# Performance work log

Measured on AMD Instinct MI355X. Metric: run time of the kernel, lower is better.

Reference implementation:

```python
import jax, jax.numpy as jnp
import numpy as np

B, T, D, U = 32, 512, 512, 512  # batch, seq_len, input dim, lstm units


def setup_inputs() -> dict:
    key = jax.random.key(0)
    ks = jax.random.split(key, 8)
    s_in = 1.0 / np.sqrt(D)
    s_rec = 1.0 / np.sqrt(U)
    return {
        "x": jax.random.normal(ks[0], (B, T, D), dtype=jnp.float32),
        "z": jax.random.normal(ks[1], (B, U), dtype=jnp.float32) * 0.1,
        # forward-direction LSTM params (Keras gate order: i, f, c, o)
        "Wf": jax.random.normal(ks[2], (D, 4 * U), dtype=jnp.float32) * s_in,
        "Uf": jax.random.normal(ks[3], (U, 4 * U), dtype=jnp.float32) * s_rec,
        "bf": jnp.zeros((4 * U,), dtype=jnp.float32),
        # backward-direction LSTM params
        "Wb": jax.random.normal(ks[4], (D, 4 * U), dtype=jnp.float32) * s_in,
        "Ub": jax.random.normal(ks[5], (U, 4 * U), dtype=jnp.float32) * s_rec,
        "bb": jnp.zeros((4 * U,), dtype=jnp.float32),
    }


def _lstm(x, h0, c0, W, Uw, b, reverse):
    """Single-direction LSTM, return_sequences=True. Keras gate order i,f,c,o."""
    u = h0.shape[-1]
    # precompute input projections for all timesteps in one big GEMM
    xg = jnp.einsum("btd,dk->btk", x, W) + b  # [B,T,4U]

    def step(carry, xg_t):
        h, c = carry
        g = xg_t + h @ Uw  # [B,4U]
        i = jax.nn.sigmoid(g[:, :u])
        f = jax.nn.sigmoid(g[:, u:2 * u])
        cc = jnp.tanh(g[:, 2 * u:3 * u])
        o = jax.nn.sigmoid(g[:, 3 * u:])
        c = f * c + i * cc
        h = o * jnp.tanh(c)
        return (h, c), h

    # scan over time; reverse=True == Keras go_backwards + output re-reversal
    _, hs = jax.lax.scan(step, (h0, c0), jnp.swapaxes(xg, 0, 1), reverse=reverse)
    return jnp.swapaxes(hs, 0, 1)  # [B,T,U]


def reference(x, z, Wf, Uf, bf, Wb, Ub, bb):
    # conditional=True: initial_state = [z, z, z, z] -> both directions get (h0=z, c0=z)
    fwd = _lstm(x, z, z, Wf, Uf, bf, reverse=False)
    bwd = _lstm(x, z, z, Wb, Ub, bb, reverse=True)
    return fwd + bwd  # Bidirectional merge_mode='sum', return_sequences=True
```

## Files before the change

### kernel.cpp

```cpp
#include <hip/hip_runtime.h>
#include <hip/hip_bf16.h>


typedef __attribute__((ext_vector_type(8))) __bf16 bf16x8;
typedef __attribute__((ext_vector_type(4))) __bf16 bf16x4;
typedef __attribute__((ext_vector_type(4))) float fvec4;

#define AS_G(p) ((const __attribute__((address_space(1))) void*)(p))
#define AS_L(p) ((__attribute__((address_space(3))) void*)(p))

__device__ __forceinline__ float sigm(float x) {
  return __builtin_amdgcn_rcpf(1.f + __expf(-x));
}
__device__ __forceinline__ float tanh_f(float x) {
  return 1.f - 2.f * __builtin_amdgcn_rcpf(__expf(2.f * x) + 1.f);
}

__device__ __forceinline__ void st_h4(__bf16* p, float h0, float h1) {
  union { __bf16 h[2]; unsigned int u; } pk;
  pk.h[0] = (__bf16)h0;
  pk.h[1] = (__bf16)h1;
  __hip_atomic_store((unsigned int*)p, pk.u, __ATOMIC_RELAXED, __HIP_MEMORY_SCOPE_AGENT);
}


__global__ void k_convert_x(const float* __restrict__ x, __bf16* __restrict__ xb) {
  size_t i = ((size_t)blockIdx.x * 256 + threadIdx.x) * 8;
  fvec4 a = *(const fvec4*)(x + i);
  fvec4 b = *(const fvec4*)(x + i + 4);
  bf16x8 o;
#pragma unroll
  for (int j = 0; j < 4; ++j) { o[j] = (__bf16)a[j]; o[4 + j] = (__bf16)b[j]; }
  *(bf16x8*)(xb + i) = o;
}

__global__ void k_build_T(const float* __restrict__ src, const float* __restrict__ bvec,
                          __bf16* __restrict__ dst, float* __restrict__ bias_out) {
  int p = blockIdx.x;
  int g = p >> 6, r = p & 63, w = r >> 4, q = r & 15, jj = q >> 2, gate = q & 3;
  int orig = gate * 512 + g * 16 + w * 4 + jj;
  for (int k = threadIdx.x; k < 512; k += 256)
    dst[(size_t)p * 512 + k] = (__bf16)src[(size_t)k * 2048 + orig];
  if (bias_out && threadIdx.x == 0) bias_out[p] = bvec[orig];
}

__global__ void k_init_flags(int* mbox) {
  int i = blockIdx.x * 256 + threadIdx.x;
  if (i < 2048) mbox[i] = 0;
}

__global__ void k_init_h(const float* __restrict__ z, __bf16* __restrict__ hbuf) {
  int idx = blockIdx.x * 256 + threadIdx.x;
  int dir = idx >> 14, rem = idx & 16383;
  int ks = rem >> 10, row = (rem >> 5) & 31, c = rem & 31;
  hbuf[(size_t)dir * 32768 + rem] = (__bf16)z[row * 512 + ks * 32 + c];
}


__global__ __launch_bounds__(256, 2) void k_gemm_xw(
    const __bf16* __restrict__ A,
    const __bf16* __restrict__ Bt,
    const float* __restrict__ bias,
    __bf16* __restrict__ C)
{
  __shared__ __align__(16) __bf16 As[128 * 32];
  __shared__ __align__(16) __bf16 Bs[128 * 32];
  const int tid = threadIdx.x;
  const int w = tid >> 6, lane = tid & 63, quad = lane >> 4, l15 = lane & 15;
  const int m0 = blockIdx.y * 128, n0 = blockIdx.x * 128;
  const int wm = w & 1, wn = w >> 1;

  fvec4 acc[4][4];
  const fvec4 zero = {0.f, 0.f, 0.f, 0.f};
#pragma unroll
  for (int i = 0; i < 4; ++i)
#pragma unroll
    for (int j = 0; j < 4; ++j) acc[i][j] = zero;

  for (int kb = 0; kb < 16; ++kb) {
    const int k0 = kb * 32;
#pragma unroll
    for (int i = 0; i < 2; ++i) {
      const int c = (i * 4 + w) * 64 + lane;
      const int row = c >> 2, kk = (c & 3) * 8;
      __builtin_amdgcn_global_load_lds(AS_G(A + (size_t)(m0 + row) * 512 + k0 + kk),
                                       AS_L(As + (size_t)(i * 4 + w) * 512), 16, 0, 0);
      __builtin_amdgcn_global_load_lds(AS_G(Bt + (size_t)(n0 + row) * 512 + k0 + kk),
                                       AS_L(Bs + (size_t)(i * 4 + w) * 512), 16, 0, 0);
    }
    __syncthreads();
    bf16x8 af[4], bfr[4];
#pragma unroll
    for (int mt = 0; mt < 4; ++mt)
      af[mt] = *(const bf16x8*)(As + (wm * 64 + mt * 16 + l15) * 32 + quad * 8);
#pragma unroll
    for (int nt = 0; nt < 4; ++nt)
      bfr[nt] = *(const bf16x8*)(Bs + (wn * 64 + nt * 16 + l15) * 32 + quad * 8);
#pragma unroll
    for (int mt = 0; mt < 4; ++mt)
#pragma unroll
      for (int nt = 0; nt < 4; ++nt)
        acc[mt][nt] = __builtin_amdgcn_mfma_f32_16x16x32_bf16(af[mt], bfr[nt], acc[mt][nt], 0, 0, 0);
    __syncthreads();
  }

#pragma unroll
  for (int nt = 0; nt < 4; ++nt) {
    const int col = n0 + wn * 64 + nt * 16 + l15;
    const float bv = bias[col];
#pragma unroll
    for (int mt = 0; mt < 4; ++mt) {
      const int rowb = m0 + wm * 64 + mt * 16 + quad * 4;
#pragma unroll
      for (int r = 0; r < 4; ++r)
        C[(size_t)(rowb + r) * 4096 + col] = (__bf16)(acc[mt][nt][r] + bv);
    }
  }
}


__global__ __launch_bounds__(256, 1) void k_lstm_rec(
    const __bf16* __restrict__ xg,
    const float* __restrict__ z,
    const __bf16* __restrict__ UT,
    __bf16* __restrict__ hbuf,
    float* __restrict__ outf,
    __bf16* __restrict__ outb,
    int* __restrict__ mbox)
{
  const int blk = blockIdx.x, dir = blk >> 5, g = blk & 31;
  const int tid = threadIdx.x, w = tid >> 6, lane = tid & 63;
  const int quad = lane >> 4, l15 = lane & 15;
  __shared__ __align__(16) __bf16 h_lds[16384];
  __shared__ __align__(16) float gates[32][68];

  bf16x8 breg[16];
  {
    const __bf16* up = UT + ((size_t)dir * 2048 + g * 64 + w * 16 + l15) * 512 + quad * 8;
#pragma unroll
    for (int ks = 0; ks < 16; ++ks) breg[ks] = *(const bf16x8*)(up + ks * 32);
  }

  const int b = lane >> 1, jpair = lane & 1;
  const int hcol = g * 16 + w * 4 + jpair * 2;
  float c0 = z[b * 512 + hcol];
  float c1 = z[b * 512 + hcol + 1];
  const __bf16* hsrc = hbuf + (size_t)dir * 32768;
  const int stoff = (g >> 1) * 1024 + b * 32 + (g & 1) * 16 + w * 4 + jpair * 2;
  const int stage_off = w * 4096 + lane * 8;
  const int swz8 = ((lane & 3) ^ ((lane >> 3) & 3)) * 8;
  const int fr_swz = ((l15 >> 1) & 3);
  int* my_line = mbox + dir * 1024 + g * 32;
  int* my_col  = mbox + dir * 1024 + lane * 32 + g;
  const fvec4 zero = {0.f, 0.f, 0.f, 0.f};

  for (int kt = 0; kt < 512; ++kt) {
    const int t = dir ? (511 - kt) : kt;
    const int pr = kt & 1;

    const bf16x8 xv = *(const bf16x8*)(xg + (size_t)(b * 512 + t) * 4096 +
                                       dir * 2048 + g * 64 + w * 16 + jpair * 8);

    if (kt > 0) {
      if (w == 0) {
        const int* mb = my_line + (lane & 31);
        for (;;) {
          int v = __hip_atomic_load(mb, __ATOMIC_RELAXED, __HIP_MEMORY_SCOPE_AGENT);
          if (!__ballot(lane < 32 && v < kt)) break;
          __builtin_amdgcn_s_sleep(1);
        }
      }
      __syncthreads();
    }

    {
      const unsigned long long* src =
          (const unsigned long long*)(hsrc + pr * 16384 + stage_off);
      unsigned long long tmp[16];
#pragma unroll
      for (int it = 0; it < 8; ++it) {
        tmp[2 * it]     = __hip_atomic_load(src + it * 128,
                            __ATOMIC_RELAXED, __HIP_MEMORY_SCOPE_AGENT);
        tmp[2 * it + 1] = __hip_atomic_load(src + it * 128 + 1,
                            __ATOMIC_RELAXED, __HIP_MEMORY_SCOPE_AGENT);
      }
#pragma unroll
      for (int it = 0; it < 8; ++it) {
        union { unsigned long long u[2]; bf16x8 v; } cv;
        cv.u[0] = tmp[2 * it];
        cv.u[1] = tmp[2 * it + 1];
        *(bf16x8*)(h_lds + (w * 4 + (it >> 1)) * 1024 +
                   ((it & 1) * 16 + (lane >> 2)) * 32 + swz8) = cv.v;
      }
    }
    __syncthreads();

    fvec4 acc0 = zero, acc1 = zero;
#pragma unroll 8
    for (int ks = 0; ks < 16; ++ks) {
      bf16x8 a0 = *(const bf16x8*)(h_lds + ks * 1024 + l15 * 32 +
                                   ((quad ^ fr_swz) * 8));
      bf16x8 a1 = *(const bf16x8*)(h_lds + ks * 1024 + (16 + l15) * 32 +
                                   ((quad ^ fr_swz) * 8));
      acc0 = __builtin_amdgcn_mfma_f32_16x16x32_bf16(a0, breg[ks], acc0, 0, 0, 0);
      acc1 = __builtin_amdgcn_mfma_f32_16x16x32_bf16(a1, breg[ks], acc1, 0, 0, 0);
    }

#pragma unroll
    for (int r = 0; r < 4; ++r) {
      gates[quad * 4 + r][w * 16 + l15] = acc0[r];
      gates[16 + quad * 4 + r][w * 16 + l15] = acc1[r];
    }
    const fvec4 gA = *(const fvec4*)&gates[b][w * 16 + jpair * 8];
    const fvec4 gB = *(const fvec4*)&gates[b][w * 16 + jpair * 8 + 4];

    float xf[8];
#pragma unroll
    for (int j = 0; j < 8; ++j) xf[j] = (float)xv[j];

    float ii = sigm(gA[0] + xf[0]);
    float ff = sigm(gA[1] + xf[1]);
    float cc = tanh_f(gA[2] + xf[2]);
    float oo = sigm(gA[3] + xf[3]);
    c0 = ff * c0 + ii * cc;
    const float h0 = oo * tanh_f(c0);

    ii = sigm(gB[0] + xf[4]);
    ff = sigm(gB[1] + xf[5]);
    cc = tanh_f(gB[2] + xf[6]);
    oo = sigm(gB[3] + xf[7]);
    c1 = ff * c1 + ii * cc;
    const float h1 = oo * tanh_f(c1);

    st_h4(hbuf + (size_t)dir * 32768 + ((kt + 1) & 1) * 16384 + stoff, h0, h1);

    __syncthreads();
    if (w == 0 && lane < 32)
      __hip_atomic_store(my_col, kt + 1, __ATOMIC_RELAXED, __HIP_MEMORY_SCOPE_AGENT);

    const size_t oidx = (size_t)(b * 512 + t) * 512 + hcol;
    if (dir == 0) {
      outf[oidx] = h0;
      outf[oidx + 1] = h1;
    } else {
      outb[oidx] = (__bf16)h0;
      outb[oidx + 1] = (__bf16)h1;
    }
  }
}


__global__ void k_add_bwd(float* __restrict__ out, const __bf16* __restrict__ outb) {
  size_t i = ((size_t)blockIdx.x * 256 + threadIdx.x) * 4;
  if (i >= (size_t)32 * 512 * 512) return;
  fvec4 o = *(const fvec4*)(out + i);
  bf16x4 bv = *(const bf16x4*)(outb + i);
#pragma unroll
  for (int j = 0; j < 4; ++j) o[j] += (float)bv[j];
  *(fvec4*)(out + i) = o;
}


extern "C" void kernel_launch(void* const* d_in, const int* in_sizes, int n_in,
                              void* d_out, int out_size, void* d_ws, size_t ws_size,
                              hipStream_t stream) {
  const float* x  = (const float*)d_in[0];
  const float* z  = (const float*)d_in[1];
  const float* Wf = (const float*)d_in[2];
  const float* Uf = (const float*)d_in[3];
  const float* bf = (const float*)d_in[4];
  const float* Wb = (const float*)d_in[5];
  const float* Ub = (const float*)d_in[6];
  const float* bb = (const float*)d_in[7];
  float* out = (float*)d_out;
  char* ws = (char*)d_ws;

  size_t off = 0;
  __bf16* xg    = (__bf16*)(ws + off); off += (size_t)16384 * 4096 * 2;
  __bf16* UT    = (__bf16*)(ws + off); off += (size_t)2 * 2048 * 512 * 2;
  __bf16* hbuf  = (__bf16*)(ws + off); off += (size_t)2 * 2 * 16384 * 2;
  int*    mbox  = (int*)(ws + off);    off += 8192;
  float*  biasp = (float*)(ws + off);  off += 4096 * 4;
  char* uni = ws + off;
  __bf16* xb   = (__bf16*)uni;
  __bf16* WT   = (__bf16*)(uni + (size_t)16384 * 512 * 2);
  __bf16* outb = (__bf16*)uni;

  k_convert_x<<<4096, 256, 0, stream>>>(x, xb);
  k_build_T<<<2048, 256, 0, stream>>>(Wf, bf, WT, biasp);
  k_build_T<<<2048, 256, 0, stream>>>(Wb, bb, WT + (size_t)2048 * 512, biasp + 2048);
  k_build_T<<<2048, 256, 0, stream>>>(Uf, nullptr, UT, nullptr);
  k_build_T<<<2048, 256, 0, stream>>>(Ub, nullptr, UT + (size_t)2048 * 512, nullptr);
  k_init_flags<<<8, 256, 0, stream>>>(mbox);
  k_init_h<<<128, 256, 0, stream>>>(z, hbuf);
  k_gemm_xw<<<dim3(32, 128), 256, 0, stream>>>(xb, WT, biasp, xg);
  k_lstm_rec<<<64, 256, 0, stream>>>(xg, z, UT, hbuf, out, outb, mbox);
  k_add_bwd<<<8192, 256, 0, stream>>>(out, outb);
}
```

Measured before the change: 2.205 ms.

## Replace mailbox flag barrier with poison-value data-driven sync on triple-buffered h

Measured after the change: 2.667 ms. +21.0%, slower.

```diff
diff --git a/kernel.cpp b/kernel.cpp
--- a/kernel.cpp
+++ b/kernel.cpp
@@ -9,6 +9,8 @@
 #define AS_G(p) ((const __attribute__((address_space(1))) void*)(p))
 #define AS_L(p) ((__attribute__((address_space(3))) void*)(p))
 
+#define POISON32 0x7F807F80u
+
 __device__ __forceinline__ float sigm(float x) {
   return __builtin_amdgcn_rcpf(1.f + __expf(-x));
 }
@@ -16,11 +18,14 @@
   return 1.f - 2.f * __builtin_amdgcn_rcpf(__expf(2.f * x) + 1.f);
 }
 
+__device__ __forceinline__ void st_u32(unsigned int* p, unsigned int v) {
+  __hip_atomic_store(p, v, __ATOMIC_RELAXED, __HIP_MEMORY_SCOPE_AGENT);
+}
 __device__ __forceinline__ void st_h4(__bf16* p, float h0, float h1) {
   union { __bf16 h[2]; unsigned int u; } pk;
   pk.h[0] = (__bf16)h0;
   pk.h[1] = (__bf16)h1;
-  __hip_atomic_store((unsigned int*)p, pk.u, __ATOMIC_RELAXED, __HIP_MEMORY_SCOPE_AGENT);
+  st_u32((unsigned int*)p, pk.u);
 }
 
 
@@ -44,16 +49,14 @@
   if (bias_out && threadIdx.x == 0) bias_out[p] = bvec[orig];
 }
 
-__global__ void k_init_flags(int* mbox) {
-  int i = blockIdx.x * 256 + threadIdx.x;
-  if (i < 2048) mbox[i] = 0;
-}
-
 __global__ void k_init_h(const float* __restrict__ z, __bf16* __restrict__ hbuf) {
   int idx = blockIdx.x * 256 + threadIdx.x;
-  int dir = idx >> 14, rem = idx & 16383;
-  int ks = rem >> 10, row = (rem >> 5) & 31, c = rem & 31;
-  hbuf[(size_t)dir * 32768 + rem] = (__bf16)z[row * 512 + ks * 32 + c];
+  int dir = idx / 49152, rem = idx % 49152;
+  int slot = rem >> 14, e = rem & 16383;
+  int ks = e >> 10, row = (e >> 5) & 31, c = e & 31;
+  union { unsigned short u; __bf16 h; } pz; pz.u = 0x7F80;
+  hbuf[(size_t)dir * 49152 + rem] =
+      (slot == 0) ? (__bf16)z[row * 512 + ks * 32 + c] : pz.h;
 }
 
 
@@ -125,8 +128,7 @@
     const __bf16* __restrict__ UT,
     __bf16* __restrict__ hbuf,
     float* __restrict__ outf,
-    __bf16* __restrict__ outb,
-    int* __restrict__ mbox)
+    __bf16* __restrict__ outb)
 {
   const int blk = blockIdx.x, dir = blk >> 5, g = blk & 31;
   const int tid = threadIdx.x, w = tid >> 6, lane = tid & 63;
@@ -145,53 +147,52 @@
   const int hcol = g * 16 + w * 4 + jpair * 2;
   float c0 = z[b * 512 + hcol];
   float c1 = z[b * 512 + hcol + 1];
-  const __bf16* hsrc = hbuf + (size_t)dir * 32768;
+  __bf16* hbase = hbuf + (size_t)dir * 49152;
   const int stoff = (g >> 1) * 1024 + b * 32 + (g & 1) * 16 + w * 4 + jpair * 2;
   const int stage_off = w * 4096 + lane * 8;
   const int swz8 = ((lane & 3) ^ ((lane >> 3) & 3)) * 8;
   const int fr_swz = ((l15 >> 1) & 3);
-  int* my_line = mbox + dir * 1024 + g * 32;
-  int* my_col  = mbox + dir * 1024 + lane * 32 + g;
   const fvec4 zero = {0.f, 0.f, 0.f, 0.f};
 
   for (int kt = 0; kt < 512; ++kt) {
     const int t = dir ? (511 - kt) : kt;
-    const int pr = kt & 1;
+    const int slot_r = kt % 3, slot_w = (kt + 1) % 3, slot_p = (kt + 2) % 3;
 
     const bf16x8 xv = *(const bf16x8*)(xg + (size_t)(b * 512 + t) * 4096 +
                                        dir * 2048 + g * 64 + w * 16 + jpair * 8);
 
-    if (kt > 0) {
-      if (w == 0) {
-        const int* mb = my_line + (lane & 31);
-        for (;;) {
-          int v = __hip_atomic_load(mb, __ATOMIC_RELAXED, __HIP_MEMORY_SCOPE_AGENT);
-          if (!__ballot(lane < 32 && v < kt)) break;
-          __builtin_amdgcn_s_sleep(1);
-        }
-      }
-      __syncthreads();
-    }
-
+    unsigned long long tmp[16];
     {
       const unsigned long long* src =
-          (const unsigned long long*)(hsrc + pr * 16384 + stage_off);
-      unsigned long long tmp[16];
-#pragma unroll
-      for (int it = 0; it < 8; ++it) {
-        tmp[2 * it]     = __hip_atomic_load(src + it * 128,
-                            __ATOMIC_RELAXED, __HIP_MEMORY_SCOPE_AGENT);
-        tmp[2 * it + 1] = __hip_atomic_load(src + it * 128 + 1,
-                            __ATOMIC_RELAXED, __HIP_MEMORY_SCOPE_AGENT);
-      }
-#pragma unroll
-      for (int it = 0; it < 8; ++it) {
-        union { unsigned long long u[2]; bf16x8 v; } cv;
-        cv.u[0] = tmp[2 * it];
-        cv.u[1] = tmp[2 * it + 1];
-        *(bf16x8*)(h_lds + (w * 4 + (it >> 1)) * 1024 +
-                   ((it & 1) * 16 + (lane >> 2)) * 32 + swz8) = cv.v;
-      }
+          (const unsigned long long*)(hbase + slot_r * 16384 + stage_off);
+      bool dirty;
+      do {
+#pragma unroll
+        for (int it = 0; it < 8; ++it) {
+          tmp[2 * it]     = __hip_atomic_load(src + it * 128,
+                              __ATOMIC_RELAXED, __HIP_MEMORY_SCOPE_AGENT);
+          tmp[2 * it + 1] = __hip_atomic_load(src + it * 128 + 1,
+                              __ATOMIC_RELAXED, __HIP_MEMORY_SCOPE_AGENT);
+        }
+        dirty = false;
+#pragma unroll
+        for (int j = 0; j < 16; ++j) {
+          dirty |= ((unsigned int)tmp[j] == POISON32);
+          dirty |= ((unsigned int)(tmp[j] >> 32) == POISON32);
+        }
+      } while (dirty);
+    }
+
+    if (kt < 511)
+      st_u32((unsigned int*)(hbase + slot_p * 16384 + stoff), POISON32);
+
+#pragma unroll
+    for (int it = 0; it < 8; ++it) {
+      union { unsigned long long u[2]; bf16x8 v; } cv;
+      cv.u[0] = tmp[2 * it];
+      cv.u[1] = tmp[2 * it + 1];
+      *(bf16x8*)(h_lds + (w * 4 + (it >> 1)) * 1024 +
+                 ((it & 1) * 16 + (lane >> 2)) * 32 + swz8) = cv.v;
     }
     __syncthreads();
 
@@ -232,11 +233,8 @@
     c1 = ff * c1 + ii * cc;
     const float h1 = oo * tanh_f(c1);
 
-    st_h4(hbuf + (size_t)dir * 32768 + ((kt + 1) & 1) * 16384 + stoff, h0, h1);
-
-    __syncthreads();
-    if (w == 0 && lane < 32)
-      __hip_atomic_store(my_col, kt + 1, __ATOMIC_RELAXED, __HIP_MEMORY_SCOPE_AGENT);
+    if (kt < 511)
+      st_h4(hbase + slot_w * 16384 + stoff, h0, h1);
 
     const size_t oidx = (size_t)(b * 512 + t) * 512 + hcol;
     if (dir == 0) {
@@ -246,6 +244,8 @@
       outb[oidx] = (__bf16)h0;
       outb[oidx + 1] = (__bf16)h1;
     }
+
+    __syncthreads();
   }
 }
 
@@ -278,8 +278,7 @@
   size_t off = 0;
   __bf16* xg    = (__bf16*)(ws + off); off += (size_t)16384 * 4096 * 2;
   __bf16* UT    = (__bf16*)(ws + off); off += (size_t)2 * 2048 * 512 * 2;
-  __bf16* hbuf  = (__bf16*)(ws + off); off += (size_t)2 * 2 * 16384 * 2;
-  int*    mbox  = (int*)(ws + off);    off += 8192;
+  __bf16* hbuf  = (__bf16*)(ws + off); off += (size_t)2 * 3 * 16384 * 2;
   float*  biasp = (float*)(ws + off);  off += 4096 * 4;
   char* uni = ws + off;
   __bf16* xb   = (__bf16*)uni;
@@ -291,9 +290,8 @@
   k_build_T<<<2048, 256, 0, stream>>>(Wb, bb, WT + (size_t)2048 * 512, biasp + 2048);
   k_build_T<<<2048, 256, 0, stream>>>(Uf, nullptr, UT, nullptr);
   k_build_T<<<2048, 256, 0, stream>>>(Ub, nullptr, UT + (size_t)2048 * 512, nullptr);
-  k_init_flags<<<8, 256, 0, stream>>>(mbox);
-  k_init_h<<<128, 256, 0, stream>>>(z, hbuf);
+  k_init_h<<<384, 256, 0, stream>>>(z, hbuf);
   k_gemm_xw<<<dim3(32, 128), 256, 0, stream>>>(xb, WT, biasp, xg);
-  k_lstm_rec<<<64, 256, 0, stream>>>(xg, z, UT, hbuf, out, outb, mbox);
+  k_lstm_rec<<<64, 256, 0, stream>>>(xg, z, UT, hbuf, out, outb);
   k_add_bwd<<<8192, 256, 0, stream>>>(out, outb);
 }
```
